# Optimization experiments

Hardware: AMD Instinct MI355X
Metric: run time of the kernel (lower is better)

## Reference

```python
import jax, jax.numpy as jnp
import numpy as np

M = 8      # number of modalities (len(ModalityType))
D = 256    # embedding_dim
B = 8192   # batch size


def setup_inputs() -> dict:
    key = jax.random.key(0)
    ks = jax.random.split(key, 12)
    s = 1.0 / np.sqrt(D)
    x = jax.random.normal(ks[0], (M, B, D), dtype=jnp.float32)
    reasoning_query = jax.random.normal(ks[1], (B, D), dtype=jnp.float32)
    # Per ordered modality pair (src, tgt): seq_len=1 MHA reduces to out_proj(V_proj(tgt)).
    Wv = jax.random.normal(ks[2], (M, M, D, D), dtype=jnp.float32) * s
    bv = jnp.zeros((M, M, D), dtype=jnp.float32)
    Wo = jax.random.normal(ks[3], (M, M, D, D), dtype=jnp.float32) * s
    bo = jnp.zeros((M, M, D), dtype=jnp.float32)
    # Per-modality fusion MLP: Linear(2D->D), ReLU, Linear(D->D)  (dropout = eval/identity)
    W1 = jax.random.normal(ks[4], (M, D, 2 * D), dtype=jnp.float32) * s
    b1 = jnp.zeros((M, D), dtype=jnp.float32)
    W2 = jax.random.normal(ks[5], (M, D, D), dtype=jnp.float32) * s
    b2 = jnp.zeros((M, D), dtype=jnp.float32)
    # Attention controller: Linear(2D->D), ReLU, Linear(D->1), Sigmoid
    Wc1 = jax.random.normal(ks[6], (D, 2 * D), dtype=jnp.float32) * s
    bc1 = jnp.zeros((D,), dtype=jnp.float32)
    wc2 = jax.random.normal(ks[7], (D,), dtype=jnp.float32) * s
    bc2 = jnp.zeros((1,), dtype=jnp.float32)
    return dict(x=x, reasoning_query=reasoning_query, Wv=Wv, bv=bv, Wo=Wo, bo=bo,
                W1=W1, b1=b1, W2=W2, b2=b2, Wc1=Wc1, bc1=bc1, wc2=wc2, bc2=bc2)


def reference(x, reasoning_query, Wv, bv, Wo, bo, W1, b1, W2, b2, Wc1, bc1, wc2, bc2):
    m = x.shape[0]
    # Cross-modal attention with seq_len=1: softmax over one key == 1, so the
    # attended output is exactly out_proj(V_proj(tgt_embedding)) for every pair.
    h = jnp.einsum('tbd,sted->stbe', x, Wv) + bv[:, :, None, :]          # [M,M,B,D]
    ctx = jnp.einsum('stbe,stoe->stbo', h, Wo) + bo[:, :, None, :]       # [M,M,B,D]
    # Mean over the M-1 target modalities (src != tgt), matching stack(...).mean(-1)
    offdiag = (1.0 - jnp.eye(m, dtype=x.dtype))[:, :, None, None]
    cross = (ctx * offdiag).sum(axis=1) / (m - 1)                         # [M,B,D]
    # Per-modality fusion MLP on cat([original, cross])
    comb = jnp.concatenate([x, cross], axis=-1)                           # [M,B,2D]
    hid = jax.nn.relu(jnp.einsum('mbf,mdf->mbd', comb, W1) + b1[:, None, :])
    fused = jnp.einsum('mbd,mod->mbo', hid, W2) + b2[:, None, :]          # [M,B,D]
    # Reasoning-query gating controller
    q = jnp.broadcast_to(reasoning_query[None], fused.shape)              # [M,B,D]
    qc = jnp.concatenate([q, fused], axis=-1)                             # [M,B,2D]
    ch = jax.nn.relu(jnp.einsum('mbf,df->mbd', qc, Wc1) + bc1)
    score = jax.nn.sigmoid(jnp.einsum('mbd,d->mb', ch, wc2) + bc2)        # [M,B]
    gated = fused * score[..., None]
    unified = gated.mean(axis=0)                                          # [B,D]
    return unified
```

## Files before the change

### kernel.cpp

```cpp
#include <hip/hip_runtime.h>

#define MMOD 8
#define BB 8192
#define DD 256

typedef unsigned short u16;
typedef __attribute__((ext_vector_type(8))) short s16x8;
typedef __attribute__((ext_vector_type(4))) float f32x4;
typedef __attribute__((ext_vector_type(8))) unsigned short u16x8;
typedef __attribute__((ext_vector_type(4))) unsigned short u16x4;
typedef __attribute__((ext_vector_type(4))) short s16x4;

typedef __attribute__((address_space(3))) unsigned short lds_u16;
typedef __attribute__((address_space(1))) const unsigned short gl_u16;

__device__ __forceinline__ float b2f(u16 u){ union{unsigned i; float f;} x; x.i=((unsigned)u)<<16; return x.f; }
__device__ __forceinline__ u16 f2b(float f){ union{float f; unsigned i;} x; x.f=f; unsigned r = x.i + 0x7FFF + ((x.i>>16)&1u); return (u16)(r>>16); }

__device__ __forceinline__ void async_cp16(const u16* g, u16* l){
  __builtin_amdgcn_global_load_lds((gl_u16*)g, (lds_u16*)l, 16, 0, 0);
}

__device__ __forceinline__ s16x8 load8_f32(const float* p, long long idx){
  float4 lo = *(const float4*)(p + idx);
  float4 hi = *(const float4*)(p + idx + 4);
  s16x8 r;
  r[0]=(short)f2b(lo.x); r[1]=(short)f2b(lo.y); r[2]=(short)f2b(lo.z); r[3]=(short)f2b(lo.w);
  r[4]=(short)f2b(hi.x); r[5]=(short)f2b(hi.y); r[6]=(short)f2b(hi.z); r[7]=(short)f2b(hi.w);
  return r;
}

struct PrepArgs {
  const float* src[10];
  u16*         dst[10];
  int          n[10];
  const float* bc2;
  float*       bc2f;
  const float* Wo;
  const float* Wv;
  u16*         WB;
  const float* bv;
  const float* bo;
  float*       cb;
};
__global__ __launch_bounds__(256, 3) void prep_kernel(PrepArgs a){
  alignas(16) __shared__ u16 lA[128*64];
  alignas(16) __shared__ u16 lB[128*64];
  const int tid = threadIdx.x;
  const unsigned bxg = blockIdx.x;

  if (bxg < 1024){
    const long long stride = 1024LL * 256LL;
    const long long base   = (long long)bxg * 256 + tid;
    if (base == 0) a.bc2f[0] = a.bc2[0];
    for (int s = 0; s < 10; s++){
      const int n  = a.n[s];
      const int n8 = n >> 3;
      const float* sp = a.src[s];
      u16* dst = a.dst[s];
      for (long long i = base; i < n8; i += stride){
        float4 lo = ((const float4*)sp)[i*2];
        float4 hi = ((const float4*)sp)[i*2+1];
        u16x8 p;
        p[0]=f2b(lo.x); p[1]=f2b(lo.y); p[2]=f2b(lo.z); p[3]=f2b(lo.w);
        p[4]=f2b(hi.x); p[5]=f2b(hi.y); p[6]=f2b(hi.z); p[7]=f2b(hi.w);
        *(u16x8*)(dst + (i<<3)) = p;
      }
      for (long long i = ((long long)n8<<3) + base; i < n; i += stride)
        dst[i] = f2b(sp[i]);
    }
  } else if (bxg < 1280){
    const int f  = (int)bxg - 1024;
    const int bwx = f & 1, bwy = (f >> 1) & 1, z = f >> 2;
    const int s = z >> 3, t = z & 7;
    if (s == t) return;
    const long long zoff = (long long)z * 65536;
    const int lane = tid & 63;
    const int w    = tid >> 6;

    f32x4 acc[4][4];
    #pragma unroll
    for (int i=0;i<4;i++)
      #pragma unroll
      for (int j=0;j<4;j++)
        #pragma unroll
        for (int r=0;r<4;r++) acc[i][j][r] = 0.0f;

    const int wr = (w >> 1) * 64, wc = (w & 1) * 64;
    const int fm = lane & 15;
    const int fk = (lane >> 4) * 8;

    int srow[4], sq[4];
    #pragma unroll
    for (int i=0;i<4;i++){
      int c = i*256 + tid;
      srow[i] = c >> 3;
      sq[i]   = (c & 7) ^ (srow[i] & 7);
    }

    for (int k0 = 0; k0 < 256; k0 += 64){
      s16x8 va[4], vt[4];
      #pragma unroll
      for (int i=0;i<4;i++){
        long long aidx = zoff + (long long)(bwx*128 + srow[i]) * 256 + k0 + sq[i]*8;
        va[i] = load8_f32(a.Wo, aidx);
      }
      #pragma unroll
      for (int j=0;j<4;j++){
        int id = j*256 + tid;
        int e  = id >> 4;
        int dc = (id & 15) * 8;
        long long bidx = zoff + (long long)(k0 + e) * 256 + bwy*128 + dc;
        vt[j] = load8_f32(a.Wv, bidx);
      }
      __syncthreads();
      #pragma unroll
      for (int i=0;i<4;i++){
        int c = i*256 + tid;
        *(s16x8*)(lA + c*8) = va[i];
      }
      #pragma unroll
      for (int j=0;j<4;j++){
        int id = j*256 + tid;
        int e  = id >> 4;
        int dc = (id & 15) * 8;
        #pragma unroll
        for (int u=0; u<8; u++){
          int d = dc + u;
          lB[(d*8 + ((e>>3) ^ (d & 7)))*8 + (e & 7)] = (u16)vt[j][u];
        }
      }
      __syncthreads();
      #pragma unroll
      for (int kk = 0; kk < 64; kk += 32){
        s16x8 af[4], bfr[4];
        const int qf = (kk + fk) >> 3;
        #pragma unroll
        for (int mi=0; mi<4; mi++){
          int r = wr + mi*16 + fm;
          af[mi] = *(const s16x8*)(lA + (r*8 + (qf ^ (r & 7))) * 8);
        }
        #pragma unroll
        for (int ni=0; ni<4; ni++){
          int r = wc + ni*16 + fm;
          bfr[ni] = *(const s16x8*)(lB + (r*8 + (qf ^ (r & 7))) * 8);
        }
        #pragma unroll
        for (int mi=0; mi<4; mi++)
          #pragma unroll
          for (int ni=0; ni<4; ni++)
            acc[mi][ni] = __builtin_amdgcn_mfma_f32_16x16x32_bf16(af[mi], bfr[ni], acc[mi][ni], 0, 0, 0);
      }
      __syncthreads();
    }
    #pragma unroll
    for (int mi=0; mi<4; mi++){
      #pragma unroll
      for (int ni=0; ni<4; ni++){
        int d = bwy*128 + wc + ni*16 + fm;
        #pragma unroll
        for (int r=0; r<4; r++){
          int o = bwx*128 + wr + mi*16 + (lane>>4)*4 + r;
          a.WB[(long long)(s*256 + o) * 2048 + t*256 + d] = f2b(acc[mi][ni][r]);
        }
      }
    }
  } else {
    const int f = (int)bxg - 1280;
    const int s = f >> 2, chunk = f & 3;
    const int lane = tid & 63, wv = tid >> 6;
    float pp[16];
    #pragma unroll
    for (int i=0;i<16;i++) pp[i] = 0.0f;
    #pragma unroll
    for (int t2 = 0; t2 < 8; t2++){
      if (t2 == s) continue;
      const int z = s*8 + t2;
      float4 bvv = *(const float4*)(a.bv + (long long)z*256 + lane*4);
      #pragma unroll
      for (int i=0;i<16;i++){
        int row = chunk*64 + wv*16 + i;
        float4 w4 = *(const float4*)(a.Wo + (long long)z*65536 + (long long)row*256 + lane*4);
        pp[i] += w4.x*bvv.x + w4.y*bvv.y + w4.z*bvv.z + w4.w*bvv.w;
      }
    }
    #pragma unroll
    for (int i=0;i<16;i++){
      #pragma unroll
      for (int off=32; off>0; off>>=1) pp[i] += __shfl_xor(pp[i], off);
    }
    if (lane == 0){
      #pragma unroll
      for (int i=0;i<16;i++){
        int row = chunk*64 + wv*16 + i;
        float bos = 0.0f;
        #pragma unroll
        for (int t2=0; t2<8; t2++){
          if (t2 == s) continue;
          bos += a.bo[(long long)(s*8+t2)*256 + row];
        }
        a.cb[s*256 + row] = (pp[i] + bos) * (1.0f/7.0f);
      }
    }
  }
}

struct GArgs {
  const u16* A;  long long a_z; long long a_piece; int lda;
  const u16* A2; long long a2_z;
  const u16* B;  long long b_z; int ldb;
  u16*       C;  long long c_z; long long c_npiece; int ldc;
  const u16* bias; long long bias_z;
  const float* cbias;
  float scale;
  int K;
  int relu;
};

__global__ __launch_bounds__(512, 2) void gemm_8ph(GArgs g){
  alignas(16) __shared__ u16 L[65536];
  const int tid  = threadIdx.x;
  const int lane = tid & 63;
  const int w    = tid >> 6;

  const int wr  = w >> 2;
  const int wcn = w & 3;
  const int fm  = lane & 15;
  const int fq  = lane >> 4;

  const long long arow0 = (long long)blockIdx.x * 256;
  const long long nrow0 = (long long)blockIdx.y * 256;
  const int ny4 = (int)blockIdx.y * 4;

  const int r0  = tid >> 3;
  const int r1  = r0 + 64;
  const int cs  = tid & 7;
  const int gc0 = cs ^ (r0 & 7);
  const int gc1 = cs ^ (r1 & 7);
  const int ldst0 = (w * 64) * 8;
  const int ldst1 = (512 + w * 64) * 8;

  const u16* Az = g.A;
  const u16* Bz = g.B;

  const long long gA0 = (arow0 + r0) * 256  + gc0 * 8;
  const long long gA1 = (arow0 + r1) * 256  + gc1 * 8;
  const long long gB0 = (nrow0 + r0) * 2048 + gc0 * 8;
  const long long gB1 = (nrow0 + r1) * 2048 + gc1 * 8;

#define MAPK(j) ((((j) >= ny4) ? (j) + 4 : (j)) << 6)

#define STAGE_A8(c, k0s, h) do{ \
    const u16* gb_ = Az + (long long)((k0s) >> 8) * 2097152LL + ((k0s) & 255) + (long long)(h) * 32768LL; \
    u16* lb_ = L + ((c) * 2 + 0) * 16384 + (h) * 8192; \
    async_cp16(gb_ + gA0, lb_ + ldst0); \
    async_cp16(gb_ + gA1, lb_ + ldst1); \
  }while(0)
#define STAGE_B8(c, k0s, h) do{ \
    const u16* gb_ = Bz + (k0s) + (long long)(h) * 262144LL; \
    u16* lb_ = L + ((c) * 2 + 1) * 16384 + (h) * 8192; \
    async_cp16(gb_ + gB0, lb_ + ldst0); \
    async_cp16(gb_ + gB1, lb_ + ldst1); \
  }while(0)

  f32x4 acc[8][4];
  #pragma unroll
  for (int i=0;i<8;i++)
    #pragma unroll
    for (int j=0;j<4;j++)
      #pragma unroll
      for (int r=0;r<4;r++) acc[i][j][r] = 0.0f;

  STAGE_A8(0, MAPK(0), 0);  STAGE_A8(0, MAPK(0), 1);
  STAGE_B8(0, MAPK(0), 0);  STAGE_B8(0, MAPK(0), 1);
  STAGE_B8(1, MAPK(1), 0);  STAGE_B8(1, MAPK(1), 1);
  asm volatile("s_waitcnt vmcnt(4)" ::: "memory");
  __builtin_amdgcn_s_barrier();

#define TILE8(cc, k0n1, k0n2, v1, v2) do{ \
    const u16* lA_ = L + ((cc) * 2 + 0) * 16384; \
    const u16* lB_ = L + ((cc) * 2 + 1) * 16384; \
    s16x8 bf[4][2]; \
    _Pragma("unroll") \
    for (int q = 0; q < 4; ++q){ \
      if (q == 0 && (v1)) STAGE_A8((cc) ^ 1, (k0n1), 0); \
      if (q == 1 && (v1)) STAGE_A8((cc) ^ 1, (k0n1), 1); \
      if (q == 2 && (v2)) STAGE_B8((cc), (k0n2), 0); \
      if (q == 3 && (v2)) STAGE_B8((cc), (k0n2), 1); \
      if (q == 0){ \
        _Pragma("unroll") \
        for (int ni = 0; ni < 4; ni++){ \
          const int R = wcn * 64 + ni * 16 + fm; \
          _Pragma("unroll") \
          for (int kk = 0; kk < 2; kk++){ \
            const int qf = kk * 4 + fq; \
            bf[ni][kk] = *(const s16x8*)(lB_ + R * 64 + ((qf ^ (R & 7)) << 3)); \
          } \
        } \
      } \
      s16x8 af[2][2]; \
      _Pragma("unroll") \
      for (int j = 0; j < 2; j++){ \
        const int R = wr * 128 + (q * 2 + j) * 16 + fm; \
        _Pragma("unroll") \
        for (int kk = 0; kk < 2; kk++){ \
          const int qf = kk * 4 + fq; \
          af[j][kk] = *(const s16x8*)(lA_ + R * 64 + ((qf ^ (R & 7)) << 3)); \
        } \
      } \
      __builtin_amdgcn_s_barrier(); \
      __builtin_amdgcn_s_setprio(1); \
      _Pragma("unroll") \
      for (int kk = 0; kk < 2; kk++) \
        _Pragma("unroll") \
        for (int j = 0; j < 2; j++) \
          _Pragma("unroll") \
          for (int ni = 0; ni < 4; ni++) \
            acc[q*2+j][ni] = __builtin_amdgcn_mfma_f32_16x16x32_bf16(af[j][kk], bf[ni][kk], acc[q*2+j][ni], 0, 0, 0); \
      __builtin_amdgcn_s_setprio(0); \
      if (q == 3){ \
        if (v2)      asm volatile("s_waitcnt vmcnt(4)" ::: "memory"); \
        else if (v1) asm volatile("s_waitcnt vmcnt(0)" ::: "memory"); \
      } \
      __builtin_amdgcn_s_barrier(); \
    } \
  }while(0)

  #pragma unroll 1
  for (int j = 0; j < 28; j += 2){
    TILE8(0, MAPK(j+1), MAPK(j+2), (j+1) < 28, (j+2) < 28);
    TILE8(1, MAPK(j+2), MAPK(j+3), (j+2) < 28, (j+3) < 28);
  }

  u16* Cb = g.C;
  #pragma unroll
  for (int mi = 0; mi < 8; mi++){
    #pragma unroll
    for (int ni = 0; ni < 4; ni++){
      const int n = (int)nrow0 + wcn * 64 + ni * 16 + fm;
      float bb = g.cbias ? g.cbias[n] : 0.0f;
      const long long cn = ((long long)(n >> 8)) * 2097152LL + (n & 255);
      #pragma unroll
      for (int r = 0; r < 4; r++){
        const long long b = arow0 + wr * 128 + mi * 16 + fq * 4 + r;
        float v = acc[mi][ni][r] * g.scale + bb;
        Cb[cn + b * 256] = f2b(v);
      }
    }
  }
#undef STAGE_A8
#undef STAGE_B8
#undef TILE8
#undef MAPK
}

__global__ __launch_bounds__(256, 4) void gemm_thin(GArgs g){
  alignas(16) __shared__ u16 lA[64*64];
  alignas(16) __shared__ u16 lB[256*64];
  const int tid  = threadIdx.x;
  const int lane = tid & 63;
  const int w    = tid >> 6;
  const int z    = blockIdx.z;

  const u16* Bbase = g.B + (long long)z * g.b_z;

  f32x4 acc[16];
  #pragma unroll
  for (int j=0;j<16;j++)
    #pragma unroll
    for (int r=0;r<4;r++) acc[j][r] = 0.0f;

  const int fm = lane & 15;
  const int fk = (lane >> 4) * 8;
  const long long arow0 = (long long)blockIdx.x * 64;

  const int sr = lane >> 3;
  const int sq = (lane & 7) ^ sr;

  for (int k0 = 0; k0 < g.K; k0 += 64){
    const u16* Abase0 = (g.A2 && k0 >= 256) ? (g.A2 + (long long)z * g.a2_z)
                                            : (g.A  + (long long)z * g.a_z);
    const u16* At = Abase0 + (long long)(k0 >> 8) * g.a_piece + (k0 & 255);
    const u16* Bt = Bbase + k0;
    __syncthreads();
    #pragma unroll
    for (int i=0;i<2;i++){
      int r = i*32 + w*8 + sr;
      async_cp16(At + (arow0 + r) * (long long)g.lda + sq*8, lA + (i*256 + w*64) * 8);
    }
    #pragma unroll
    for (int i=0;i<8;i++){
      int r = i*32 + w*8 + sr;
      async_cp16(Bt + (long long)r * g.ldb + sq*8, lB + (i*256 + w*64) * 8);
    }
    __syncthreads();
    #pragma unroll
    for (int kk = 0; kk < 64; kk += 32){
      const int qf = (kk + fk) >> 3;
      int ra = w*16 + fm;
      s16x8 af = *(const s16x8*)(lA + (ra*8 + (qf ^ (ra & 7))) * 8);
      #pragma unroll
      for (int ni=0; ni<16; ni++){
        int r = ni*16 + fm;
        s16x8 bfr = *(const s16x8*)(lB + (r*8 + (qf ^ (r & 7))) * 8);
        acc[ni] = __builtin_amdgcn_mfma_f32_16x16x32_bf16(af, bfr, acc[ni], 0, 0, 0);
      }
    }
  }

  u16* Cb = g.C + (long long)z * g.c_z;
  const u16* biasp = g.bias ? g.bias + (long long)z * g.bias_z : (const u16*)0;
  #pragma unroll
  for (int ni=0; ni<16; ni++){
    int n = ni*16 + fm;
    float bb = 0.0f;
    if (g.cbias) bb = g.cbias[n];
    else if (biasp) bb = b2f(biasp[n]);
    #pragma unroll
    for (int r=0; r<4; r++){
      long long b = arow0 + w*16 + (lane>>4)*4 + r;
      float v = acc[ni][r] * g.scale + bb;
      if (g.relu) v = v > 0.0f ? v : 0.0f;
      Cb[b * (long long)g.ldc + n] = f2b(v);
    }
  }
}

struct S34Args {
  const u16* X;
  const u16* CR;
  const u16* W1;
  const u16* W2;
  const u16* Wc1h;
  const u16* b1;
  const u16* b2;
  const u16* bc1;
  const u16* wc2;
  const u16* qctx;
  const float* bc2f;
  float*     scores;
  u16*       F;
};
__global__ __launch_bounds__(256, 2) void gemm_s345(S34Args a){
  alignas(16) __shared__ u16 lB[256*64];
  alignas(16) __shared__ u16 lH[64*256];
  u16* lA = lH;

  const int tid  = threadIdx.x;
  const int lane = tid & 63;
  const int w    = tid >> 6;
  const int z    = blockIdx.z;

  const int fm = lane & 15;
  const int fq = lane >> 4;
  const long long arow0 = (long long)blockIdx.x * 64;
  const long long BD = (long long)BB * DD;

  const int sr = lane >> 3;
  const int sq = (lane & 7) ^ sr;

  const u16* Xz  = a.X  + (long long)z * BD;
  const u16* CRz = a.CR + (long long)z * BD;
  const u16* W1z = a.W1 + (long long)z * 131072;
  const u16* W2z = a.W2 + (long long)z * 65536;

  f32x4 acc[16];
  #pragma unroll
  for (int j=0;j<16;j++)
    #pragma unroll
    for (int r=0;r<4;r++) acc[j][r] = 0.0f;

  for (int k0 = 0; k0 < 512; k0 += 64){
    const u16* At = (k0 < 256) ? (Xz + k0) : (CRz + (k0 - 256));
    const u16* Bt = W1z + k0;
    __syncthreads();
    #pragma unroll
    for (int i=0;i<2;i++){
      int r = i*32 + w*8 + sr;
      async_cp16(At + (arow0 + r) * 256 + sq*8, lA + (i*256 + w*64) * 8);
    }
    #pragma unroll
    for (int i=0;i<8;i++){
      int r = i*32 + w*8 + sr;
      async_cp16(Bt + (long long)r * 512 + sq*8, lB + (i*256 + w*64) * 8);
    }
    __syncthreads();
    #pragma unroll
    for (int kk = 0; kk < 64; kk += 32){
      const int qf = (kk >> 3) + fq;
      int ra = w*16 + fm;
      s16x8 af = *(const s16x8*)(lA + (ra*8 + (qf ^ (ra & 7))) * 8);
      #pragma unroll
      for (int ni=0; ni<16; ni++){
        int r = ni*16 + fm;
        s16x8 bfr = *(const s16x8*)(lB + (r*8 + (qf ^ (r & 7))) * 8);
        acc[ni] = __builtin_amdgcn_mfma_f32_16x16x32_bf16(bfr, af, acc[ni], 0, 0, 0);
      }
    }
  }

  __syncthreads();

  {
    const int b = w*16 + fm;
    #pragma unroll
    for (int ni=0; ni<16; ni++){
      s16x4 b1v = *(const s16x4*)(a.b1 + (long long)z*256 + ni*16 + fq*4);
      u16x4 pk;
      #pragma unroll
      for (int r=0; r<4; r++){
        float v = acc[ni][r] + b2f((u16)b1v[r]);
        v = v > 0.0f ? v : 0.0f;
        pk[r] = f2b(v);
      }
      const int c = ni*2 + (fq >> 1);
      const int csw = (c & ~7) | ((c & 7) ^ (b & 7));
      *(u16x4*)(lH + b*256 + csw*8 + (fq & 1)*4) = pk;
    }
  }

  f32x4 acc2[16];
  #pragma unroll
  for (int j=0;j<16;j++)
    #pragma unroll
    for (int r=0;r<4;r++) acc2[j][r] = 0.0f;

  for (int k0 = 0; k0 < 256; k0 += 64){
    const u16* Bt = W2z + k0;
    __syncthreads();
    #pragma unroll
    for (int i=0;i<8;i++){
      int r = i*32 + w*8 + sr;
      async_cp16(Bt + (long long)r * 256 + sq*8, lB + (i*256 + w*64) * 8);
    }
    __syncthreads();
    #pragma unroll
    for (int kk = 0; kk < 64; kk += 32){
      const int ra = w*16 + fm;
      const int qa = ((k0 + kk) >> 3) + fq;
      const int qsw = (qa & ~7) | ((qa & 7) ^ (ra & 7));
      s16x8 af = *(const s16x8*)(lH + ra*256 + qsw*8);
      const int qf = (kk >> 3) + fq;
      #pragma unroll
      for (int ni=0; ni<16; ni++){
        int r = ni*16 + fm;
        s16x8 bfr = *(const s16x8*)(lB + (r*8 + (qf ^ (r & 7))) * 8);
        acc2[ni] = __builtin_amdgcn_mfma_f32_16x16x32_bf16(bfr, af, acc2[ni], 0, 0, 0);
      }
    }
  }

  __syncthreads();

  {
    const int b = w*16 + fm;
    u16* Fz = a.F + (long long)z * BD;
    #pragma unroll
    for (int ni=0; ni<16; ni++){
      s16x4 b2v = *(const s16x4*)(a.b2 + (long long)z*256 + ni*16 + fq*4);
      u16x4 pk;
      #pragma unroll
      for (int r=0; r<4; r++)
        pk[r] = f2b(acc2[ni][r] + b2f((u16)b2v[r]));
      *(u16x4*)(Fz + (arow0 + b)*256 + ni*16 + fq*4) = pk;
      const int c = ni*2 + (fq >> 1);
      const int csw = (c & ~7) | ((c & 7) ^ (b & 7));
      *(u16x4*)(lH + b*256 + csw*8 + (fq & 1)*4) = pk;
    }
  }

  f32x4 acc3[16];
  #pragma unroll
  for (int j=0;j<16;j++)
    #pragma unroll
    for (int r=0;r<4;r++) acc3[j][r] = 0.0f;

  for (int k0 = 0; k0 < 256; k0 += 64){
    const u16* Bt = a.Wc1h + k0;
    __syncthreads();
    #pragma unroll
    for (int i=0;i<8;i++){
      int r = i*32 + w*8 + sr;
      async_cp16(Bt + (long long)r * 512 + sq*8, lB + (i*256 + w*64) * 8);
    }
    __syncthreads();
    #pragma unroll
    for (int kk = 0; kk < 64; kk += 32){
      const int ra = w*16 + fm;
      const int qa = ((k0 + kk) >> 3) + fq;
      const int qsw = (qa & ~7) | ((qa & 7) ^ (ra & 7));
      s16x8 af = *(const s16x8*)(lH + ra*256 + qsw*8);
      const int qf = (kk >> 3) + fq;
      #pragma unroll
      for (int ni=0; ni<16; ni++){
        int r = ni*16 + fm;
        s16x8 bfr = *(const s16x8*)(lB + (r*8 + (qf ^ (r & 7))) * 8);
        acc3[ni] = __builtin_amdgcn_mfma_f32_16x16x32_bf16(af, bfr, acc3[ni], 0, 0, 0);
      }
    }
  }

  float p[4] = {0.f, 0.f, 0.f, 0.f};
  #pragma unroll
  for (int ni=0; ni<16; ni++){
    int n = ni*16 + fm;
    float bb = b2f(a.bc1[n]);
    float wcv = b2f(a.wc2[n]);
    #pragma unroll
    for (int r=0; r<4; r++){
      long long b = arow0 + w*16 + fq*4 + r;
      float v = acc3[ni][r] + bb + b2f(a.qctx[b*256 + n]);
      v = v > 0.0f ? v : 0.0f;
      p[r] += v * wcv;
    }
  }
  #pragma unroll
  for (int r=0; r<4; r++){
    #pragma unroll
    for (int off=1; off<16; off<<=1) p[r] += __shfl_xor(p[r], off);
  }
  if (fm == 0){
    float bc2v = a.bc2f[0];
    #pragma unroll
    for (int r=0; r<4; r++){
      long long b = arow0 + w*16 + fq*4 + r;
      a.scores[(long long)z*BB + b] = 1.0f / (1.0f + __expf(-(p[r] + bc2v)));
    }
  }
}

__global__ __launch_bounds__(256) void final_gate(const u16* fused, const float* scores, float* out){
  const int tid = threadIdx.x;
  for (int b = blockIdx.x; b < BB; b += gridDim.x){
    float acc = 0.0f;
    #pragma unroll
    for (int m=0; m<8; m++)
      acc += b2f(fused[((long long)m*BB + b)*256 + tid]) * scores[(long long)m*BB + b];
    out[(long long)b*256 + tid] = acc * 0.125f;
  }
}

extern "C" void kernel_launch(void* const* d_in, const int* in_sizes, int n_in,
                              void* d_out, int out_size, void* d_ws, size_t ws_size,
                              hipStream_t stream){
  const float* x   = (const float*)d_in[0];
  const float* q   = (const float*)d_in[1];
  const float* Wv  = (const float*)d_in[2];
  const float* bv  = (const float*)d_in[3];
  const float* Wo  = (const float*)d_in[4];
  const float* bo  = (const float*)d_in[5];
  const float* W1  = (const float*)d_in[6];
  const float* b1  = (const float*)d_in[7];
  const float* W2  = (const float*)d_in[8];
  const float* b2  = (const float*)d_in[9];
  const float* Wc1 = (const float*)d_in[10];
  const float* bc1 = (const float*)d_in[11];
  const float* wc2 = (const float*)d_in[12];
  const float* bc2 = (const float*)d_in[13];

  char* ws = (char*)d_ws;
  u16*   xb    = (u16*)(ws + 0LL);
  u16*   qb    = (u16*)(ws + 33554432LL);
  u16*   cross = (u16*)(ws + 37748736LL);
  u16*   WB    = (u16*)(ws + 104857600LL);
  u16*   W1b   = (u16*)(ws + 113246208LL);
  u16*   W2b   = (u16*)(ws + 115343360LL);
  u16*   Wc1b  = (u16*)(ws + 116391936LL);
  u16*   b1b   = (u16*)(ws + 116654080LL);
  u16*   b2b   = (u16*)(ws + 116658176LL);
  u16*   bc1b  = (u16*)(ws + 116662272LL);
  u16*   wc2b  = (u16*)(ws + 116662784LL);
  float* bc2f  = (float*)(ws + 116663296LL);
  float* cb    = (float*)(ws + 116663424LL);
  u16*   fused = xb;
  u16*   qctx  = WB;
  float* scores = (float*)(ws + 104857600LL + 4194304LL);

  PrepArgs pa{};
  pa.src[0]=x;   pa.dst[0]=xb;   pa.n[0]=MMOD*BB*DD;
  pa.src[1]=q;   pa.dst[1]=qb;   pa.n[1]=BB*DD;
  pa.src[2]=W1;  pa.dst[2]=W1b;  pa.n[2]=MMOD*DD*2*DD;
  pa.src[3]=W2;  pa.dst[3]=W2b;  pa.n[3]=MMOD*DD*DD;
  pa.src[4]=Wc1; pa.dst[4]=Wc1b; pa.n[4]=DD*2*DD;
  pa.src[5]=b1;  pa.dst[5]=b1b;  pa.n[5]=MMOD*DD;
  pa.src[6]=b2;  pa.dst[6]=b2b;  pa.n[6]=MMOD*DD;
  pa.src[7]=bc1; pa.dst[7]=bc1b; pa.n[7]=DD;
  pa.src[8]=wc2; pa.dst[8]=wc2b; pa.n[8]=DD;
  pa.src[9]=bc2; pa.dst[9]=bc1b; pa.n[9]=0;
  pa.bc2 = bc2; pa.bc2f = bc2f;
  pa.Wo = Wo; pa.Wv = Wv; pa.WB = WB;
  pa.bv = bv; pa.bo = bo; pa.cb = cb;
  prep_kernel<<<1312, 256, 0, stream>>>(pa);

  const long long BD = (long long)BB * DD;

  GArgs g2{};
  g2.A = xb; g2.a_z = 0; g2.a_piece = BD; g2.lda = 256; g2.A2 = 0; g2.a2_z = 0;
  g2.B = WB; g2.b_z = 0; g2.ldb = 2048;
  g2.C = cross; g2.c_z = 0; g2.c_npiece = BD; g2.ldc = 256;
  g2.bias = 0; g2.bias_z = 0; g2.cbias = cb;
  g2.scale = 1.0f/7.0f; g2.K = 2048; g2.relu = 0;
  gemm_8ph<<<dim3(32,8,1), 512, 0, stream>>>(g2);

  GArgs g5a{};
  g5a.A = qb; g5a.a_z = 0; g5a.a_piece = 0; g5a.lda = 256; g5a.A2 = 0; g5a.a2_z = 0;
  g5a.B = Wc1b; g5a.b_z = 0; g5a.ldb = 512;
  g5a.C = qctx; g5a.c_z = 0; g5a.c_npiece = 0; g5a.ldc = 256;
  g5a.bias = 0; g5a.bias_z = 0; g5a.cbias = 0;
  g5a.scale = 1.0f; g5a.K = 256; g5a.relu = 0;
  gemm_thin<<<dim3(128,1,1), 256, 0, stream>>>(g5a);

  S34Args s34{};
  s34.X = xb; s34.CR = cross; s34.W1 = W1b; s34.W2 = W2b; s34.Wc1h = Wc1b + 256;
  s34.b1 = b1b; s34.b2 = b2b; s34.bc1 = bc1b; s34.wc2 = wc2b;
  s34.qctx = qctx; s34.bc2f = bc2f; s34.scores = scores; s34.F = fused;
  gemm_s345<<<dim3(128,1,8), 256, 0, stream>>>(s34);

  final_gate<<<dim3(1024), 256, 0, stream>>>(fused, scores, (float*)d_out);

  (void)in_sizes; (void)n_in; (void)out_size; (void)ws_size;
}
```

Measured before the change: 316.8 us.

## Fuse query-controller GEMM into prep kernel and double-buffer s345 first GEMM

Removes the separate gemm_thin launch by computing q·Wc1[:, :256] inside extra prep_kernel blocks, reading fp32 q and Wc1 directly and converting to bf16 in registers, which also drops the bf16 copy of q. Separately, the W1 stage of gemm_s345 is reworked into a two-buffer software pipeline so global-to-LDS loads for the next K tile overlap MFMA on the current tile. It needs extra LDS (a second A buffer, and the prep lB doubled), which may lower occupancy. qctx moves to its own workspace region since it no longer aliases WB.

```diff
diff --git a/kernel.cpp b/kernel.cpp
--- a/kernel.cpp
+++ b/kernel.cpp
@@ -42,10 +42,13 @@
   const float* bv;
   const float* bo;
   float*       cb;
+  const float* q;
+  const float* Wc1f;
+  u16*         qctx;
 };
 __global__ __launch_bounds__(256, 3) void prep_kernel(PrepArgs a){
   alignas(16) __shared__ u16 lA[128*64];
-  alignas(16) __shared__ u16 lB[128*64];
+  alignas(16) __shared__ u16 lB[256*64];
   const int tid = threadIdx.x;
   const unsigned bxg = blockIdx.x;
 
@@ -165,7 +168,7 @@
         }
       }
     }
-  } else {
+  } else if (bxg < 1312){
     const int f = (int)bxg - 1280;
     const int s = f >> 2, chunk = f & 3;
     const int lane = tid & 63, wv = tid >> 6;
@@ -200,6 +203,71 @@
           bos += a.bo[(long long)(s*8+t2)*256 + row];
         }
         a.cb[s*256 + row] = (pp[i] + bos) * (1.0f/7.0f);
+      }
+    }
+  } else {
+    const int f = (int)bxg - 1312;
+    const long long brow0 = (long long)f * 64;
+    const int lane = tid & 63;
+    const int w    = tid >> 6;
+    const int fm = lane & 15;
+    const int fk = (lane >> 4) * 8;
+
+    f32x4 acc[16];
+    #pragma unroll
+    for (int j=0;j<16;j++)
+      #pragma unroll
+      for (int r=0;r<4;r++) acc[j][r] = 0.0f;
+
+    for (int k0 = 0; k0 < 256; k0 += 64){
+      s16x8 va[2], vb[8];
+      #pragma unroll
+      for (int i=0;i<2;i++){
+        int c = i*256 + tid;
+        int r = c >> 3, cs = c & 7;
+        int gq = cs ^ (r & 7);
+        va[i] = load8_f32(a.q, (brow0 + r) * 256 + k0 + gq*8);
+      }
+      #pragma unroll
+      for (int j=0;j<8;j++){
+        int c = j*256 + tid;
+        int r = c >> 3, cs = c & 7;
+        int gq = cs ^ (r & 7);
+        vb[j] = load8_f32(a.Wc1f, (long long)r * 512 + k0 + gq*8);
+      }
+      __syncthreads();
+      #pragma unroll
+      for (int i=0;i<2;i++){
+        int c = i*256 + tid;
+        *(s16x8*)(lA + c*8) = va[i];
+      }
+      #pragma unroll
+      for (int j=0;j<8;j++){
+        int c = j*256 + tid;
+        *(s16x8*)(lB + c*8) = vb[j];
+      }
+      __syncthreads();
+      #pragma unroll
+      for (int kk = 0; kk < 64; kk += 32){
+        const int qf = (kk + fk) >> 3;
+        int ra = w*16 + fm;
+        s16x8 af = *(const s16x8*)(lA + (ra*8 + (qf ^ (ra & 7))) * 8);
+        #pragma unroll
+        for (int ni=0; ni<16; ni++){
+          int r = ni*16 + fm;
+          s16x8 bfr = *(const s16x8*)(lB + (r*8 + (qf ^ (r & 7))) * 8);
+          acc[ni] = __builtin_amdgcn_mfma_f32_16x16x32_bf16(af, bfr, acc[ni], 0, 0, 0);
+        }
+      }
+      __syncthreads();
+    }
+    #pragma unroll
+    for (int ni=0; ni<16; ni++){
+      int n = ni*16 + fm;
+      #pragma unroll
+      for (int r=0; r<4; r++){
+        long long b = brow0 + w*16 + (lane>>4)*4 + r;
+        a.qctx[b * 256 + n] = f2b(acc[ni][r]);
       }
     }
   }
@@ -354,78 +422,6 @@
 #undef MAPK
 }
 
-__global__ __launch_bounds__(256, 4) void gemm_thin(GArgs g){
-  alignas(16) __shared__ u16 lA[64*64];
-  alignas(16) __shared__ u16 lB[256*64];
-  const int tid  = threadIdx.x;
-  const int lane = tid & 63;
-  const int w    = tid >> 6;
-  const int z    = blockIdx.z;
-
-  const u16* Bbase = g.B + (long long)z * g.b_z;
-
-  f32x4 acc[16];
-  #pragma unroll
-  for (int j=0;j<16;j++)
-    #pragma unroll
-    for (int r=0;r<4;r++) acc[j][r] = 0.0f;
-
-  const int fm = lane & 15;
-  const int fk = (lane >> 4) * 8;
-  const long long arow0 = (long long)blockIdx.x * 64;
-
-  const int sr = lane >> 3;
-  const int sq = (lane & 7) ^ sr;
-
-  for (int k0 = 0; k0 < g.K; k0 += 64){
-    const u16* Abase0 = (g.A2 && k0 >= 256) ? (g.A2 + (long long)z * g.a2_z)
-                                            : (g.A  + (long long)z * g.a_z);
-    const u16* At = Abase0 + (long long)(k0 >> 8) * g.a_piece + (k0 & 255);
-    const u16* Bt = Bbase + k0;
-    __syncthreads();
-    #pragma unroll
-    for (int i=0;i<2;i++){
-      int r = i*32 + w*8 + sr;
-      async_cp16(At + (arow0 + r) * (long long)g.lda + sq*8, lA + (i*256 + w*64) * 8);
-    }
-    #pragma unroll
-    for (int i=0;i<8;i++){
-      int r = i*32 + w*8 + sr;
-      async_cp16(Bt + (long long)r * g.ldb + sq*8, lB + (i*256 + w*64) * 8);
-    }
-    __syncthreads();
-    #pragma unroll
-    for (int kk = 0; kk < 64; kk += 32){
-      const int qf = (kk + fk) >> 3;
-      int ra = w*16 + fm;
-      s16x8 af = *(const s16x8*)(lA + (ra*8 + (qf ^ (ra & 7))) * 8);
-      #pragma unroll
-      for (int ni=0; ni<16; ni++){
-        int r = ni*16 + fm;
-        s16x8 bfr = *(const s16x8*)(lB + (r*8 + (qf ^ (r & 7))) * 8);
-        acc[ni] = __builtin_amdgcn_mfma_f32_16x16x32_bf16(af, bfr, acc[ni], 0, 0, 0);
-      }
-    }
-  }
-
-  u16* Cb = g.C + (long long)z * g.c_z;
-  const u16* biasp = g.bias ? g.bias + (long long)z * g.bias_z : (const u16*)0;
-  #pragma unroll
-  for (int ni=0; ni<16; ni++){
-    int n = ni*16 + fm;
-    float bb = 0.0f;
-    if (g.cbias) bb = g.cbias[n];
-    else if (biasp) bb = b2f(biasp[n]);
-    #pragma unroll
-    for (int r=0; r<4; r++){
-      long long b = arow0 + w*16 + (lane>>4)*4 + r;
-      float v = acc[ni][r] * g.scale + bb;
-      if (g.relu) v = v > 0.0f ? v : 0.0f;
-      Cb[b * (long long)g.ldc + n] = f2b(v);
-    }
-  }
-}
-
 struct S34Args {
   const u16* X;
   const u16* CR;
@@ -444,7 +440,7 @@
 __global__ __launch_bounds__(256, 2) void gemm_s345(S34Args a){
   alignas(16) __shared__ u16 lB[256*64];
   alignas(16) __shared__ u16 lH[64*256];
-  u16* lA = lH;
+  alignas(16) __shared__ u16 lAb[2][64*64];
 
   const int tid  = threadIdx.x;
   const int lane = tid & 63;
@@ -470,36 +466,57 @@
     #pragma unroll
     for (int r=0;r<4;r++) acc[j][r] = 0.0f;
 
-  for (int k0 = 0; k0 < 512; k0 += 64){
-    const u16* At = (k0 < 256) ? (Xz + k0) : (CRz + (k0 - 256));
-    const u16* Bt = W1z + k0;
-    __syncthreads();
-    #pragma unroll
-    for (int i=0;i<2;i++){
-      int r = i*32 + w*8 + sr;
-      async_cp16(At + (arow0 + r) * 256 + sq*8, lA + (i*256 + w*64) * 8);
-    }
-    #pragma unroll
-    for (int i=0;i<8;i++){
-      int r = i*32 + w*8 + sr;
-      async_cp16(Bt + (long long)r * 512 + sq*8, lB + (i*256 + w*64) * 8);
-    }
-    __syncthreads();
-    #pragma unroll
-    for (int kk = 0; kk < 64; kk += 32){
-      const int qf = (kk >> 3) + fq;
-      int ra = w*16 + fm;
-      s16x8 af = *(const s16x8*)(lA + (ra*8 + (qf ^ (ra & 7))) * 8);
-      #pragma unroll
-      for (int ni=0; ni<16; ni++){
-        int r = ni*16 + fm;
-        s16x8 bfr = *(const s16x8*)(lB + (r*8 + (qf ^ (r & 7))) * 8);
-        acc[ni] = __builtin_amdgcn_mfma_f32_16x16x32_bf16(bfr, af, acc[ni], 0, 0, 0);
-      }
-    }
-  }
-
-  __syncthreads();
+#define STA_A(t, dst) do{ \
+    const u16* At_ = ((t) < 4) ? (Xz + (t)*64) : (CRz + ((t)-4)*64); \
+    _Pragma("unroll") \
+    for (int i=0;i<2;i++){ \
+      int r = i*32 + w*8 + sr; \
+      async_cp16(At_ + (arow0 + r) * 256 + sq*8, (dst) + (i*256 + w*64) * 8); \
+    } \
+  }while(0)
+#define STB_A(t, dst) do{ \
+    const u16* Bt_ = W1z + (t)*64; \
+    _Pragma("unroll") \
+    for (int i=0;i<8;i++){ \
+      int r = i*32 + w*8 + sr; \
+      async_cp16(Bt_ + (long long)r * 512 + sq*8, (dst) + (i*256 + w*64) * 8); \
+    } \
+  }while(0)
+#define COMPUTE_A(la, wb) do{ \
+    _Pragma("unroll") \
+    for (int kk = 0; kk < 64; kk += 32){ \
+      const int qf = (kk >> 3) + fq; \
+      int ra = w*16 + fm; \
+      s16x8 af = *(const s16x8*)((la) + (ra*8 + (qf ^ (ra & 7))) * 8); \
+      _Pragma("unroll") \
+      for (int ni=0; ni<16; ni++){ \
+        int r = ni*16 + fm; \
+        s16x8 bfr = *(const s16x8*)((wb) + (r*8 + (qf ^ (r & 7))) * 8); \
+        acc[ni] = __builtin_amdgcn_mfma_f32_16x16x32_bf16(bfr, af, acc[ni], 0, 0, 0); \
+      } \
+    } \
+  }while(0)
+
+  STA_A(0, lAb[0]);
+  STB_A(0, lB);
+  asm volatile("s_waitcnt vmcnt(0)" ::: "memory");
+  __builtin_amdgcn_s_barrier();
+
+  #pragma unroll
+  for (int tp = 0; tp < 4; tp++){
+    const int t0 = tp*2, t1 = tp*2 + 1;
+    if (t0 + 1 < 8){ STA_A(t0+1, lAb[1]); STB_A(t0+1, lH); }
+    COMPUTE_A(lAb[0], lB);
+    asm volatile("s_waitcnt vmcnt(0)" ::: "memory");
+    __builtin_amdgcn_s_barrier();
+    if (t1 + 1 < 8){ STA_A(t1+1, lAb[0]); STB_A(t1+1, lB); }
+    COMPUTE_A(lAb[1], lH);
+    asm volatile("s_waitcnt vmcnt(0)" ::: "memory");
+    __builtin_amdgcn_s_barrier();
+  }
+#undef STA_A
+#undef STB_A
+#undef COMPUTE_A
 
   {
     const int b = w*16 + fm;
@@ -660,8 +677,8 @@
 
   char* ws = (char*)d_ws;
   u16*   xb    = (u16*)(ws + 0LL);
-  u16*   qb    = (u16*)(ws + 33554432LL);
   u16*   cross = (u16*)(ws + 37748736LL);
+  u16*   qctx  = (u16*)(ws + 71303168LL);
   u16*   WB    = (u16*)(ws + 104857600LL);
   u16*   W1b   = (u16*)(ws + 113246208LL);
   u16*   W2b   = (u16*)(ws + 115343360LL);
@@ -673,12 +690,11 @@
   float* bc2f  = (float*)(ws + 116663296LL);
   float* cb    = (float*)(ws + 116663424LL);
   u16*   fused = xb;
-  u16*   qctx  = WB;
   float* scores = (float*)(ws + 104857600LL + 4194304LL);
 
   PrepArgs pa{};
   pa.src[0]=x;   pa.dst[0]=xb;   pa.n[0]=MMOD*BB*DD;
-  pa.src[1]=q;   pa.dst[1]=qb;   pa.n[1]=BB*DD;
+  pa.src[1]=x;   pa.dst[1]=xb;   pa.n[1]=0;
   pa.src[2]=W1;  pa.dst[2]=W1b;  pa.n[2]=MMOD*DD*2*DD;
   pa.src[3]=W2;  pa.dst[3]=W2b;  pa.n[3]=MMOD*DD*DD;
   pa.src[4]=Wc1; pa.dst[4]=Wc1b; pa.n[4]=DD*2*DD;
@@ -690,7 +706,8 @@
   pa.bc2 = bc2; pa.bc2f = bc2f;
   pa.Wo = Wo; pa.Wv = Wv; pa.WB = WB;
   pa.bv = bv; pa.bo = bo; pa.cb = cb;
-  prep_kernel<<<1312, 256, 0, stream>>>(pa);
+  pa.q = q; pa.Wc1f = Wc1; pa.qctx = qctx;
+  prep_kernel<<<1440, 256, 0, stream>>>(pa);
 
   const long long BD = (long long)BB * DD;
 
@@ -702,14 +719,6 @@
   g2.scale = 1.0f/7.0f; g2.K = 2048; g2.relu = 0;
   gemm_8ph<<<dim3(32,8,1), 512, 0, stream>>>(g2);
 
-  GArgs g5a{};
-  g5a.A = qb; g5a.a_z = 0; g5a.a_piece = 0; g5a.lda = 256; g5a.A2 = 0; g5a.a2_z = 0;
-  g5a.B = Wc1b; g5a.b_z = 0; g5a.ldb = 512;
-  g5a.C = qctx; g5a.c_z = 0; g5a.c_npiece = 0; g5a.ldc = 256;
-  g5a.bias = 0; g5a.bias_z = 0; g5a.cbias = 0;
-  g5a.scale = 1.0f; g5a.K = 256; g5a.relu = 0;
-  gemm_thin<<<dim3(128,1,1), 256, 0, stream>>>(g5a);
-
   S34Args s34{};
   s34.X = xb; s34.CR = cross; s34.W1 = W1b; s34.W2 = W2b; s34.Wc1h = Wc1b + 256;
   s34.b1 = b1b; s34.b2 = b2b; s34.bc1 = bc1b; s34.wc2 = wc2b;
```

Result: faster. 301.0 us (-5.0%).
